# Kernel tuning notes

Measured on AMD Instinct MI355X. Metric: run time of the kernel, lower is better.

The kernel has to match this reference:

```python
import jax, jax.numpy as jnp
import numpy as np

B, C, H, W = 32, 512, 32, 32
R = C // 2  # reduced channels for key/prod projections


def setup_inputs() -> dict:
    key = jax.random.key(0)
    ks = jax.random.split(key, 8)
    s_in = 1.0 / np.sqrt(C)
    return {
        "x": jax.random.normal(ks[0], (B, C, H, W), jnp.float32),
        "Wk": jax.random.normal(ks[1], (R, C), jnp.float32) * s_in,
        "bk": jax.random.normal(ks[2], (R,), jnp.float32) * s_in,
        "Wp": jax.random.normal(ks[3], (R, C), jnp.float32) * s_in,
        "bp": jax.random.normal(ks[4], (R,), jnp.float32) * s_in,
        "Wv": jax.random.normal(ks[5], (C, C), jnp.float32) * s_in,
        "bv": jax.random.normal(ks[6], (C,), jnp.float32) * s_in,
        "param": jax.random.normal(ks[7], (1,), jnp.float32),
    }


def _conv1x1(x, Wmat, b):
    # 1x1 conv on NCHW == per-pixel channel matmul
    return jnp.einsum('bchw,oc->bohw', x, Wmat) + b[None, :, None, None]


def reference(x, Wk, bk, Wp, bp, Wv, bv, param):
    b, c, h, w = x.shape
    hw = h * w
    f_key = _conv1x1(x, Wk, bk).reshape(b, -1, hw).transpose(0, 2, 1)  # [B,HW,R]
    f_prod = _conv1x1(x, Wp, bp).reshape(b, -1, hw)                    # [B,R,HW]
    f_value = _conv1x1(x, Wv, bv).reshape(b, -1, hw)                   # [B,C,HW]
    energy = jnp.einsum('bnr,brm->bnm', f_key, f_prod)                 # [B,HW,HW]
    similarity = jax.nn.softmax(energy, axis=-1)
    # bmm(f_value, similarity^T): out[b,c,n] = sum_m f_value[b,c,m] * sim[b,n,m]
    attended = jnp.einsum('bcm,bnm->bcn', f_value, similarity).reshape(b, c, h, w)
    return x + attended * param
```

## Files before the change

### kernel.cpp

```cpp
#include <hip/hip_runtime.h>
#include <hip/hip_bf16.h>

#define BATCH 32
#define CCH   512
#define HWSZ  1024
#define RCH   256

typedef __attribute__((ext_vector_type(8))) _Float16 f16x8;
typedef __attribute__((ext_vector_type(4))) float f32x4;

__device__ __forceinline__ ushort f2h(float f) {
    _Float16 h = (_Float16)f;
    ushort u; __builtin_memcpy(&u, &h, 2);
    return u;
}
__device__ __forceinline__ float h2f(ushort u) {
    _Float16 h; __builtin_memcpy(&h, &u, 2);
    return (float)h;
}

__device__ __forceinline__ void load_lds16(const void* g, void* l) {
    __builtin_amdgcn_global_load_lds((const __attribute__((address_space(1))) void*)g,
                                     (__attribute__((address_space(3))) void*)l,
                                     16, 0, 0);
}

__device__ __forceinline__ f32x4 mfma16(f16x8 a, f16x8 b, f32x4 c) {
    return __builtin_amdgcn_mfma_f32_16x16x32_f16(a, b, c, 0, 0, 0);
}

__device__ __forceinline__ void xcd_swizzle(int& bx, int& by, int& bz) {
    int gx = gridDim.x, gy = gridDim.y;
    int n   = gx * gy * gridDim.z;
    int lin = bx + gx * (by + gy * bz);
    int cpx = n >> 3;
    int s = (lin & 7) * cpx + (lin >> 3);
    bx = s % gx; s /= gx;
    by = s % gy;
    bz = s / gy;
}

__global__ __launch_bounds__(256) void k_pre(
    const float* __restrict__ x, ushort* __restrict__ xt,
    const float* __restrict__ Wk, const float* __restrict__ bk,
    const float* __restrict__ Wp, const float* __restrict__ bp,
    const float* __restrict__ Wv,
    ushort* __restrict__ Wkp_h, ushort* __restrict__ Wv_h, float* __restrict__ bias_kp)
{
    __shared__ float tile[64][68];
    int t = threadIdx.x;
    if (blockIdx.z == 32) {
        int base = ((blockIdx.y * 16 + blockIdx.x) * 256 + t) * 8;
        int o = base >> 9, c = base & 511;
        const float* srcKP = (o < 256) ? (Wk + (size_t)o * 512 + c)
                                       : (Wp + (size_t)(o - 256) * 512 + c);
        float4 a0 = *(const float4*)srcKP;
        float4 a1 = *(const float4*)(srcKP + 4);
        ushort4 h0, h1;
        h0.x = f2h(a0.x); h0.y = f2h(a0.y); h0.z = f2h(a0.z); h0.w = f2h(a0.w);
        h1.x = f2h(a1.x); h1.y = f2h(a1.y); h1.z = f2h(a1.z); h1.w = f2h(a1.w);
        *(ushort4*)&Wkp_h[base] = h0;
        *(ushort4*)&Wkp_h[base + 4] = h1;
        float4 v0 = *(const float4*)(Wv + base);
        float4 v1 = *(const float4*)(Wv + base + 4);
        h0.x = f2h(v0.x); h0.y = f2h(v0.y); h0.z = f2h(v0.z); h0.w = f2h(v0.w);
        h1.x = f2h(v1.x); h1.y = f2h(v1.y); h1.z = f2h(v1.z); h1.w = f2h(v1.w);
        *(ushort4*)&Wv_h[base] = h0;
        *(ushort4*)&Wv_h[base + 4] = h1;
        if (c == 0) bias_kp[o] = (o < 256) ? bk[o] : bp[o - 256];
        return;
    }
    int b  = blockIdx.z;
    int c0 = blockIdx.y * 64;
    int n0 = blockIdx.x * 64;
    const float* xb = x + (size_t)b * CCH * HWSZ;
    int tc  = t >> 4;
    int tn4 = (t & 15) * 4;
    #pragma unroll
    for (int i = 0; i < 4; ++i) {
        int c = tc + i * 16;
        *(float4*)&tile[c][tn4] = *(const float4*)&xb[(size_t)(c0 + c) * HWSZ + n0 + tn4];
    }
    __syncthreads();
    ushort* oh = xt + (size_t)b * HWSZ * CCH;
    int tn  = t >> 4;
    int tc4 = (t & 15) * 4;
    #pragma unroll
    for (int i = 0; i < 4; ++i) {
        int n = tn + i * 16;
        ushort4 h;
        h.x = f2h(tile[tc4 + 0][n]);
        h.y = f2h(tile[tc4 + 1][n]);
        h.z = f2h(tile[tc4 + 2][n]);
        h.w = f2h(tile[tc4 + 3][n]);
        *(ushort4*)&oh[(size_t)(n0 + n) * CCH + c0 + tc4] = h;
    }
}

template<int MODE>
__global__ __launch_bounds__(512, 4) void k_gemm128(
    const ushort* __restrict__ A, const ushort* __restrict__ B,
    int lda, int ldb, long aBatch, long bBatch,
    ushort* __restrict__ out16, long oBatch, int ldo,
    const float* __restrict__ bias, int NT)
{
    __shared__ ushort lds[2][12288];
    int bx = blockIdx.x, by = blockIdx.y, bz = blockIdx.z;
    xcd_swizzle(bx, by, bz);
    const int z  = bz;
    const int m0 = bx * 128;
    const int n0 = by * 256;
    const int t    = threadIdx.x;
    const int lane = t & 63;
    const int w    = t >> 6;
    const int wm = w >> 2, wn = w & 3;
    const int l15 = lane & 15;
    const int hi  = lane >> 4;
    const int G   = hi ^ ((lane >> 1) & 3);

    const ushort* Ab = A + (size_t)z * aBatch;
    const ushort* Bb = B + (size_t)z * bBatch;

    const int sr = t >> 2;
    const int sg = (t & 3) ^ ((t >> 3) & 3);

    f32x4 acc[4][4] = {};
    f16x8 a[4], b01[2], b23[2];

#define STAGE(slot, kt) do {                                                 \
        size_t sa_ = (size_t)(m0 + sr) * lda + (kt) * 32 + sg * 8;           \
        load_lds16(Ab + sa_, &lds[slot][t * 8]);                             \
        size_t sb_ = (size_t)(n0 + sr) * ldb + (kt) * 32 + sg * 8;           \
        load_lds16(Bb + sb_, &lds[slot][4096 + t * 8]);                      \
        load_lds16(Bb + sb_ + (size_t)128 * ldb, &lds[slot][8192 + t * 8]);  \
    } while (0)

#define RD_ALL(slot) do {                                                    \
        _Pragma("unroll")                                                    \
        for (int ni = 0; ni < 2; ++ni)                                       \
            b01[ni] = *(const f16x8*)&lds[slot][4096 + (wn * 64 + ni * 16 + l15) * 32 + G * 8]; \
        _Pragma("unroll")                                                    \
        for (int ni = 0; ni < 2; ++ni)                                       \
            b23[ni] = *(const f16x8*)&lds[slot][4096 + (wn * 64 + 32 + ni * 16 + l15) * 32 + G * 8]; \
        _Pragma("unroll")                                                    \
        for (int mi = 0; mi < 4; ++mi)                                       \
            a[mi] = *(const f16x8*)&lds[slot][(wm * 64 + mi * 16 + l15) * 32 + G * 8]; \
    } while (0)

#define BAR() __builtin_amdgcn_s_barrier()
#define WLG(N) do { asm volatile("s_waitcnt lgkmcnt(" #N ")" ::: "memory");  \
                    __builtin_amdgcn_sched_barrier(0); } while (0)
#define WVM(N) asm volatile("s_waitcnt vmcnt(" #N ")" ::: "memory")

#define MM4(mi) do {                                                         \
        acc[mi][0] = mfma16(a[mi], b01[0], acc[mi][0]);                      \
        acc[mi][1] = mfma16(a[mi], b01[1], acc[mi][1]);                      \
        acc[mi][2] = mfma16(a[mi], b23[0], acc[mi][2]);                      \
        acc[mi][3] = mfma16(a[mi], b23[1], acc[mi][3]);                      \
    } while (0)

#define MFMA_PIPE() do {                                                     \
        WLG(3); MM4(0); WLG(2); MM4(1); WLG(1); MM4(2); WLG(0); MM4(3);      \
    } while (0)

    STAGE(0, 0);
    WVM(0);
    BAR();
    for (int j = 0; j < NT - 1; ++j) {
        int cur = j & 1;
        STAGE(cur ^ 1, j + 1);
        RD_ALL(cur);
        MFMA_PIPE();
        WVM(0);
        BAR();
    }
    RD_ALL(1);
    MFMA_PIPE();

    #pragma unroll
    for (int mi = 0; mi < 4; ++mi) {
        #pragma unroll
        for (int ni = 0; ni < 4; ++ni) {
            int gc  = n0 + wn * 64 + (ni >> 1) * 32 + (ni & 1) * 16 + l15;
            int gr0 = m0 + wm * 64 + mi * 16 + hi * 4;
            #pragma unroll
            for (int jj = 0; jj < 4; ++jj) {
                int gr = gr0 + jj;
                float v = acc[mi][ni][jj];
                if (MODE == 0) {
                    v += bias[gc];
                    out16[(size_t)gr * ldo + gc] = f2h(v);
                } else {
                    v += bias[gr];
                    out16[(size_t)z * oBatch + (size_t)gr * ldo + gc] = f2h(v);
                }
            }
        }
    }
#undef STAGE
#undef RD_ALL
#undef BAR
#undef WLG
#undef WVM
#undef MM4
#undef MFMA_PIPE
}

template<int MODE>
__global__ __launch_bounds__(512, 2) void k_gemm256(
    const ushort* __restrict__ A, const ushort* __restrict__ B,
    int lda, int ldb, long aBatch, long bBatch,
    float* __restrict__ outF, ushort* __restrict__ out16,
    long oBatch, int ldo,
    const float* __restrict__ xres, const float* __restrict__ param,
    int NT)
{
    __shared__ ushort lds[2][2][2][8192];
    int bx = blockIdx.x, by = blockIdx.y, bz = blockIdx.z;
    xcd_swizzle(bx, by, bz);
    const int z  = bz;
    const int m0 = bx * 256;
    const int n0 = by * 256;
    const int t    = threadIdx.x;
    const int lane = t & 63;
    const int w    = t >> 6;
    const int wm = w >> 2, wn = w & 3;
    const int l15 = lane & 15;
    const int hi  = lane >> 4;
    const int G   = hi ^ ((lane >> 1) & 3);

    const ushort* Ab = A + (size_t)z * aBatch;
    const ushort* Bb = B + (size_t)z * bBatch;

    const int sr = t >> 2;
    const int sg = (t & 3) ^ ((t >> 3) & 3);

    f32x4 acc[8][4] = {};
    f16x8 a[8], b[2];

#define STAGE(par, op, ks, kt) do {                                          \
        const ushort* gb_ = (op) ? Bb : Ab;                                  \
        int ld_ = (op) ? ldb : lda;                                          \
        int r0_ = (op) ? n0 : m0;                                            \
        size_t src_ = (size_t)(r0_ + sr) * ld_ + (kt) * 64 + (ks) * 32 + sg * 8; \
        load_lds16(gb_ + src_, &lds[par][op][ks][t * 8]);                    \
        load_lds16(gb_ + src_ + (size_t)128 * ld_, &lds[par][op][ks][t * 8 + 4096]); \
    } while (0)

#define LDA_(cur, ks) do {                                                   \
        _Pragma("unroll")                                                    \
        for (int mi = 0; mi < 8; ++mi)                                       \
            a[mi] = *(const f16x8*)&lds[cur][0][ks][(wm * 128 + mi * 16 + l15) * 32 + G * 8]; \
    } while (0)

#define LDB_(cur, ks, nh) do {                                               \
        _Pragma("unroll")                                                    \
        for (int ni = 0; ni < 2; ++ni)                                       \
            b[ni] = *(const f16x8*)&lds[cur][1][ks][(wn * 64 + (nh) * 32 + ni * 16 + l15) * 32 + G * 8]; \
    } while (0)

#define BAR() __builtin_amdgcn_s_barrier()

#define WLG(N) do { asm volatile("s_waitcnt lgkmcnt(" #N ")" ::: "memory");  \
                    __builtin_amdgcn_sched_barrier(0); } while (0)

#define MM2(mi, nh) do {                                                     \
        acc[mi][(nh)*2+0] = mfma16(a[mi], b[0], acc[mi][(nh)*2+0]);          \
        acc[mi][(nh)*2+1] = mfma16(a[mi], b[1], acc[mi][(nh)*2+1]);          \
    } while (0)

#define MFMA_PIPE() do {                                                     \
        WLG(7); MM2(0, 0); WLG(6); MM2(1, 0); WLG(5); MM2(2, 0);             \
        WLG(4); MM2(3, 0); WLG(3); MM2(4, 0); WLG(2); MM2(5, 0);             \
        WLG(1); MM2(6, 0); WLG(0); MM2(7, 0);                                \
    } while (0)

#define MFMA_BLK1() do {                                                     \
        WLG(0);                                                              \
        MM2(0, 1); MM2(1, 1); MM2(2, 1); MM2(3, 1);                          \
        MM2(4, 1); MM2(5, 1); MM2(6, 1); MM2(7, 1);                          \
    } while (0)

    STAGE(0, 0, 0, 0); STAGE(0, 1, 0, 0); STAGE(0, 0, 1, 0); STAGE(0, 1, 1, 0);
    asm volatile("s_waitcnt vmcnt(4)" ::: "memory");
    BAR();

    for (int j = 0; j < NT - 1; ++j) {
        int cur = j & 1, nxt = cur ^ 1;
        STAGE(nxt, 0, 0, j + 1);
        LDB_(cur, 0, 0); LDA_(cur, 0);
        MFMA_PIPE();
        STAGE(nxt, 1, 0, j + 1);
        LDB_(cur, 0, 1);
        MFMA_BLK1();
        asm volatile("s_waitcnt vmcnt(4)" ::: "memory");
        BAR();
        STAGE(nxt, 0, 1, j + 1);
        LDB_(cur, 1, 0); LDA_(cur, 1);
        MFMA_PIPE();
        STAGE(nxt, 1, 1, j + 1);
        LDB_(cur, 1, 1);
        MFMA_BLK1();
        asm volatile("s_waitcnt vmcnt(4)" ::: "memory");
        BAR();
    }
    {
        int cur = (NT - 1) & 1;
        LDB_(cur, 0, 0); LDA_(cur, 0);
        MFMA_PIPE();
        LDB_(cur, 0, 1);
        MFMA_BLK1();
        asm volatile("s_waitcnt vmcnt(0)" ::: "memory");
        BAR();
        LDB_(cur, 1, 0); LDA_(cur, 1);
        MFMA_PIPE();
        LDB_(cur, 1, 1);
        MFMA_BLK1();
    }

    if (MODE == 3) {
        float* fbuf = (float*)lds;
        const float prm = param[0];
        float*       ob = outF + (size_t)z * oBatch;
        const float* xb = xres + (size_t)z * oBatch;
        #pragma unroll
        for (int h = 0; h < 2; ++h) {
            asm volatile("s_waitcnt lgkmcnt(0)" ::: "memory");
            BAR();
            if ((wn >> 1) == h) {
                #pragma unroll
                for (int mi = 0; mi < 8; ++mi)
                    #pragma unroll
                    for (int ni = 0; ni < 4; ++ni) {
                        int cc = (wn & 1) * 64 + (ni >> 1) * 32 + (ni & 1) * 16 + l15;
                        int nn = (wm * 128 + mi * 16 + hi * 4) ^ ((cc & 7) << 2);
                        *(f32x4*)&fbuf[cc * 256 + nn] = acc[mi][ni];
                    }
            }
            asm volatile("s_waitcnt lgkmcnt(0)" ::: "memory");
            BAR();
            #pragma unroll
            for (int rr = 0; rr < 16; ++rr) {
                int cc = w * 16 + rr;
                f32x4 o4 = *(const f32x4*)&fbuf[cc * 256 + ((lane * 4) ^ ((cc & 7) << 2))];
                size_t g = (size_t)(n0 + h * 128 + cc) * ldo + m0 + lane * 4;
                float4 xv = *(const float4*)&xb[g];
                float4 ov;
                ov.x = xv.x + o4[0] * prm;
                ov.y = xv.y + o4[1] * prm;
                ov.z = xv.z + o4[2] * prm;
                ov.w = xv.w + o4[3] * prm;
                *(float4*)&ob[g] = ov;
            }
        }
    } else {
        #pragma unroll
        for (int mi = 0; mi < 8; ++mi) {
            #pragma unroll
            for (int ni = 0; ni < 4; ++ni) {
                int gc  = n0 + wn * 64 + (ni >> 1) * 32 + (ni & 1) * 16 + l15;
                int gr0 = m0 + wm * 128 + mi * 16 + hi * 4;
                #pragma unroll
                for (int jj = 0; jj < 4; ++jj) {
                    int gr = gr0 + jj;
                    out16[(size_t)z * oBatch + (size_t)(gr0 + jj) * ldo + gc] = f2h(acc[mi][ni][jj]);
                    (void)gr;
                }
            }
        }
    }
#undef STAGE
#undef LDA_
#undef LDB_
#undef BAR
#undef WLG
#undef MM2
#undef MFMA_PIPE
#undef MFMA_BLK1
}

__global__ __launch_bounds__(256) void k_softmax(ushort* __restrict__ E)
{
    int t    = threadIdx.x;
    int rowi = t >> 7;
    int tl   = t & 127;
    ushort* row = E + (size_t)(blockIdx.x * 2 + rowi) * HWSZ;
    uint4 u = *(const uint4*)&row[tl * 8];
    float v[8];
    v[0] = h2f(u.x & 0xffff); v[1] = h2f(u.x >> 16);
    v[2] = h2f(u.y & 0xffff); v[3] = h2f(u.y >> 16);
    v[4] = h2f(u.z & 0xffff); v[5] = h2f(u.z >> 16);
    v[6] = h2f(u.w & 0xffff); v[7] = h2f(u.w >> 16);
    float mx = v[0];
    #pragma unroll
    for (int i = 1; i < 8; ++i) mx = fmaxf(mx, v[i]);
    #pragma unroll
    for (int off = 1; off < 64; off <<= 1)
        mx = fmaxf(mx, __shfl_xor(mx, off));
    __shared__ float redm[2][2];
    __shared__ float reds[2][2];
    int lane = t & 63, wv = (t >> 6) & 1;
    if (lane == 0) redm[rowi][wv] = mx;
    __syncthreads();
    mx = fmaxf(redm[rowi][0], redm[rowi][1]);
    float s = 0.f;
    #pragma unroll
    for (int i = 0; i < 8; ++i) { v[i] = __expf(v[i] - mx); s += v[i]; }
    #pragma unroll
    for (int off = 1; off < 64; off <<= 1)
        s += __shfl_xor(s, off);
    if (lane == 0) reds[rowi][wv] = s;
    __syncthreads();
    s = reds[rowi][0] + reds[rowi][1];
    float inv = 1.0f / s;
    uint4 o;
    o.x = (unsigned)f2h(v[0] * inv) | ((unsigned)f2h(v[1] * inv) << 16);
    o.y = (unsigned)f2h(v[2] * inv) | ((unsigned)f2h(v[3] * inv) << 16);
    o.z = (unsigned)f2h(v[4] * inv) | ((unsigned)f2h(v[5] * inv) << 16);
    o.w = (unsigned)f2h(v[6] * inv) | ((unsigned)f2h(v[7] * inv) << 16);
    *(uint4*)&row[tl * 8] = o;
}

extern "C" void kernel_launch(void* const* d_in, const int* in_sizes, int n_in,
                              void* d_out, int out_size, void* d_ws, size_t ws_size,
                              hipStream_t stream)
{
    const float* x    = (const float*)d_in[0];
    const float* Wk   = (const float*)d_in[1];
    const float* bk   = (const float*)d_in[2];
    const float* Wp   = (const float*)d_in[3];
    const float* bp   = (const float*)d_in[4];
    const float* Wv   = (const float*)d_in[5];
    const float* bv   = (const float*)d_in[6];
    const float* prm  = (const float*)d_in[7];
    float* out = (float*)d_out;
    char* ws = (char*)d_ws;

    const size_t SZ16 = (size_t)BATCH * HWSZ * CCH * 2;
    ushort* xt    = (ushort*)(ws + 0);
    ushort* KPt   = (ushort*)(ws + SZ16);
    ushort* fv    = (ushort*)(ws + 2 * SZ16);
    ushort* E     = (ushort*)(ws + 3 * SZ16);
    char* wbase   = ws + 3 * SZ16 + (size_t)BATCH * HWSZ * HWSZ * 2;
    ushort* Wkp_h = (ushort*)(wbase);
    ushort* Wv_h  = (ushort*)(wbase + 524288);
    float*  bias_kp = (float*)(wbase + 2 * 524288);

    k_pre<<<dim3(16, 8, 33), 256, 0, stream>>>(
        x, xt, Wk, bk, Wp, bp, Wv, Wkp_h, Wv_h, bias_kp);

    k_gemm128<0><<<dim3(256, 2, 1), 512, 0, stream>>>(
        xt, Wkp_h, CCH, CCH, 0, 0,
        KPt, 0, CCH, bias_kp, CCH / 32);

    k_gemm128<1><<<dim3(4, 4, 32), 512, 0, stream>>>(
        Wv_h, xt, CCH, CCH, 0, (long)HWSZ * CCH,
        fv, (long)CCH * HWSZ, HWSZ, bv, CCH / 32);

    k_gemm256<2><<<dim3(4, 4, 32), 512, 0, stream>>>(
        KPt, KPt + RCH, CCH, CCH,
        (long)HWSZ * CCH, (long)HWSZ * CCH,
        nullptr, E, (long)HWSZ * HWSZ, HWSZ,
        nullptr, nullptr, RCH / 64);

    k_softmax<<<BATCH * HWSZ / 2, 256, 0, stream>>>(E);

    k_gemm256<3><<<dim3(4, 2, 32), 512, 0, stream>>>(
        E, fv, HWSZ, HWSZ,
        (long)HWSZ * HWSZ, (long)CCH * HWSZ,
        out, nullptr, (long)CCH * HWSZ, HWSZ,
        x, prm, HWSZ / 64);
}
```

Measured before the change: 176.7 us.

## Merge key/prod and value projections into one launch; halve energy GEMM grid

Fuses the two projection GEMMs (key/prod and value) into one kernel launch, using blockIdx.z to pick which GEMM a block computes. This removes one launch and the tail gap between the two kernels. The energy GEMM now has each block compute two 256-wide N tiles in sequence, halving its grid so there are fewer blocks and less scheduling overhead. The cost is more serial work per block, with no reuse of the A tile across the two N tiles.

```diff
diff --git a/kernel.cpp b/kernel.cpp
--- a/kernel.cpp
+++ b/kernel.cpp
@@ -97,19 +97,15 @@
     }
 }
 
-template<int MODE>
-__global__ __launch_bounds__(512, 4) void k_gemm128(
-    const ushort* __restrict__ A, const ushort* __restrict__ B,
-    int lda, int ldb, long aBatch, long bBatch,
-    ushort* __restrict__ out16, long oBatch, int ldo,
-    const float* __restrict__ bias, int NT)
+__global__ __launch_bounds__(512, 4) void k_proj(
+    const ushort* __restrict__ xt, const ushort* __restrict__ Wkp_h,
+    const ushort* __restrict__ Wv_h, const float* __restrict__ bias_kp,
+    const float* __restrict__ bv,
+    ushort* __restrict__ KPt, ushort* __restrict__ fv)
 {
     __shared__ ushort lds[2][12288];
     int bx = blockIdx.x, by = blockIdx.y, bz = blockIdx.z;
     xcd_swizzle(bx, by, bz);
-    const int z  = bz;
-    const int m0 = bx * 128;
-    const int n0 = by * 256;
     const int t    = threadIdx.x;
     const int lane = t & 63;
     const int w    = t >> 6;
@@ -117,22 +113,37 @@
     const int l15 = lane & 15;
     const int hi  = lane >> 4;
     const int G   = hi ^ ((lane >> 1) & 3);
-
-    const ushort* Ab = A + (size_t)z * aBatch;
-    const ushort* Bb = B + (size_t)z * bBatch;
-
     const int sr = t >> 2;
     const int sg = (t & 3) ^ ((t >> 3) & 3);
+    const int NT = CCH / 32;
+
+    const ushort *Ab, *Bb;
+    ushort* outp;
+    const float* bias;
+    int m0, n0, ldo;
+    bool colB;
+    if (bz < 32) {
+        Ab = Wv_h;
+        Bb = xt + (size_t)bz * HWSZ * CCH;
+        outp = fv + (size_t)bz * CCH * HWSZ;
+        bias = bv; colB = false; ldo = HWSZ;
+        m0 = bx * 128; n0 = by * 256;
+    } else {
+        int idx = (bz - 32) * 16 + by * 4 + bx;
+        Ab = xt; Bb = Wkp_h;
+        outp = KPt; bias = bias_kp; colB = true; ldo = CCH;
+        m0 = (idx >> 1) * 128; n0 = (idx & 1) * 256;
+    }
 
     f32x4 acc[4][4] = {};
     f16x8 a[4], b01[2], b23[2];
 
 #define STAGE(slot, kt) do {                                                 \
-        size_t sa_ = (size_t)(m0 + sr) * lda + (kt) * 32 + sg * 8;           \
+        size_t sa_ = (size_t)(m0 + sr) * CCH + (kt) * 32 + sg * 8;           \
         load_lds16(Ab + sa_, &lds[slot][t * 8]);                             \
-        size_t sb_ = (size_t)(n0 + sr) * ldb + (kt) * 32 + sg * 8;           \
+        size_t sb_ = (size_t)(n0 + sr) * CCH + (kt) * 32 + sg * 8;           \
         load_lds16(Bb + sb_, &lds[slot][4096 + t * 8]);                      \
-        load_lds16(Bb + sb_ + (size_t)128 * ldb, &lds[slot][8192 + t * 8]);  \
+        load_lds16(Bb + sb_ + (size_t)128 * CCH, &lds[slot][8192 + t * 8]);  \
     } while (0)
 
 #define RD_ALL(slot) do {                                                    \
@@ -186,14 +197,8 @@
             #pragma unroll
             for (int jj = 0; jj < 4; ++jj) {
                 int gr = gr0 + jj;
-                float v = acc[mi][ni][jj];
-                if (MODE == 0) {
-                    v += bias[gc];
-                    out16[(size_t)gr * ldo + gc] = f2h(v);
-                } else {
-                    v += bias[gr];
-                    out16[(size_t)z * oBatch + (size_t)gr * ldo + gc] = f2h(v);
-                }
+                float v = acc[mi][ni][jj] + (colB ? bias[gc] : bias[gr]);
+                outp[(size_t)gr * ldo + gc] = f2h(v);
             }
         }
     }
@@ -220,7 +225,6 @@
     xcd_swizzle(bx, by, bz);
     const int z  = bz;
     const int m0 = bx * 256;
-    const int n0 = by * 256;
     const int t    = threadIdx.x;
     const int lane = t & 63;
     const int w    = t >> 6;
@@ -235,8 +239,7 @@
     const int sr = t >> 2;
     const int sg = (t & 3) ^ ((t >> 3) & 3);
 
-    f32x4 acc[8][4] = {};
-    f16x8 a[8], b[2];
+    int n0;
 
 #define STAGE(par, op, ks, kt) do {                                          \
         const ushort* gb_ = (op) ? Bb : Ab;                                  \
@@ -281,90 +284,94 @@
         MM2(4, 1); MM2(5, 1); MM2(6, 1); MM2(7, 1);                          \
     } while (0)
 
-    STAGE(0, 0, 0, 0); STAGE(0, 1, 0, 0); STAGE(0, 0, 1, 0); STAGE(0, 1, 1, 0);
-    asm volatile("s_waitcnt vmcnt(4)" ::: "memory");
-    BAR();
-
-    for (int j = 0; j < NT - 1; ++j) {
-        int cur = j & 1, nxt = cur ^ 1;
-        STAGE(nxt, 0, 0, j + 1);
-        LDB_(cur, 0, 0); LDA_(cur, 0);
-        MFMA_PIPE();
-        STAGE(nxt, 1, 0, j + 1);
-        LDB_(cur, 0, 1);
-        MFMA_BLK1();
+    const int nyN = (MODE == 2) ? 2 : 1;
+    for (int ny = 0; ny < nyN; ++ny) {
+        n0 = (MODE == 2) ? (by * 512 + ny * 256) : (by * 256);
+        f32x4 acc[8][4] = {};
+        f16x8 a[8], b[2];
+
+        STAGE(0, 0, 0, 0); STAGE(0, 1, 0, 0); STAGE(0, 0, 1, 0); STAGE(0, 1, 1, 0);
         asm volatile("s_waitcnt vmcnt(4)" ::: "memory");
         BAR();
-        STAGE(nxt, 0, 1, j + 1);
-        LDB_(cur, 1, 0); LDA_(cur, 1);
-        MFMA_PIPE();
-        STAGE(nxt, 1, 1, j + 1);
-        LDB_(cur, 1, 1);
-        MFMA_BLK1();
-        asm volatile("s_waitcnt vmcnt(4)" ::: "memory");
-        BAR();
-    }
-    {
-        int cur = (NT - 1) & 1;
-        LDB_(cur, 0, 0); LDA_(cur, 0);
-        MFMA_PIPE();
-        LDB_(cur, 0, 1);
-        MFMA_BLK1();
-        asm volatile("s_waitcnt vmcnt(0)" ::: "memory");
-        BAR();
-        LDB_(cur, 1, 0); LDA_(cur, 1);
-        MFMA_PIPE();
-        LDB_(cur, 1, 1);
-        MFMA_BLK1();
-    }
-
-    if (MODE == 3) {
-        float* fbuf = (float*)lds;
-        const float prm = param[0];
-        float*       ob = outF + (size_t)z * oBatch;
-        const float* xb = xres + (size_t)z * oBatch;
-        #pragma unroll
-        for (int h = 0; h < 2; ++h) {
-            asm volatile("s_waitcnt lgkmcnt(0)" ::: "memory");
+
+        for (int j = 0; j < NT - 1; ++j) {
+            int cur = j & 1, nxt = cur ^ 1;
+            STAGE(nxt, 0, 0, j + 1);
+            LDB_(cur, 0, 0); LDA_(cur, 0);
+            MFMA_PIPE();
+            STAGE(nxt, 1, 0, j + 1);
+            LDB_(cur, 0, 1);
+            MFMA_BLK1();
+            asm volatile("s_waitcnt vmcnt(4)" ::: "memory");
             BAR();
-            if ((wn >> 1) == h) {
+            STAGE(nxt, 0, 1, j + 1);
+            LDB_(cur, 1, 0); LDA_(cur, 1);
+            MFMA_PIPE();
+            STAGE(nxt, 1, 1, j + 1);
+            LDB_(cur, 1, 1);
+            MFMA_BLK1();
+            asm volatile("s_waitcnt vmcnt(4)" ::: "memory");
+            BAR();
+        }
+        {
+            int cur = (NT - 1) & 1;
+            LDB_(cur, 0, 0); LDA_(cur, 0);
+            MFMA_PIPE();
+            LDB_(cur, 0, 1);
+            MFMA_BLK1();
+            asm volatile("s_waitcnt vmcnt(0)" ::: "memory");
+            BAR();
+            LDB_(cur, 1, 0); LDA_(cur, 1);
+            MFMA_PIPE();
+            LDB_(cur, 1, 1);
+            MFMA_BLK1();
+        }
+
+        if (MODE == 3) {
+            float* fbuf = (float*)lds;
+            const float prm = param[0];
+            float*       ob = outF + (size_t)z * oBatch;
+            const float* xb = xres + (size_t)z * oBatch;
+            #pragma unroll
+            for (int h = 0; h < 2; ++h) {
+                asm volatile("s_waitcnt lgkmcnt(0)" ::: "memory");
+                BAR();
+                if ((wn >> 1) == h) {
+                    #pragma unroll
+                    for (int mi = 0; mi < 8; ++mi)
+                        #pragma unroll
+                        for (int ni = 0; ni < 4; ++ni) {
+                            int cc = (wn & 1) * 64 + (ni >> 1) * 32 + (ni & 1) * 16 + l15;
+                            int nn = (wm * 128 + mi * 16 + hi * 4) ^ ((cc & 7) << 2);
+                            *(f32x4*)&fbuf[cc * 256 + nn] = acc[mi][ni];
+                        }
+                }
+                asm volatile("s_waitcnt lgkmcnt(0)" ::: "memory");
+                BAR();
                 #pragma unroll
-                for (int mi = 0; mi < 8; ++mi)
+                for (int rr = 0; rr < 16; ++rr) {
+                    int cc = w * 16 + rr;
+                    f32x4 o4 = *(const f32x4*)&fbuf[cc * 256 + ((lane * 4) ^ ((cc & 7) << 2))];
+                    size_t g = (size_t)(n0 + h * 128 + cc) * ldo + m0 + lane * 4;
+                    float4 xv = *(const float4*)&xb[g];
+                    float4 ov;
+                    ov.x = xv.x + o4[0] * prm;
+                    ov.y = xv.y + o4[1] * prm;
+                    ov.z = xv.z + o4[2] * prm;
+                    ov.w = xv.w + o4[3] * prm;
+                    *(float4*)&ob[g] = ov;
+                }
+            }
+        } else {
+            #pragma unroll
+            for (int mi = 0; mi < 8; ++mi) {
+                #pragma unroll
+                for (int ni = 0; ni < 4; ++ni) {
+                    int gc  = n0 + wn * 64 + (ni >> 1) * 32 + (ni & 1) * 16 + l15;
+                    int gr0 = m0 + wm * 128 + mi * 16 + hi * 4;
                     #pragma unroll
-                    for (int ni = 0; ni < 4; ++ni) {
-                        int cc = (wn & 1) * 64 + (ni >> 1) * 32 + (ni & 1) * 16 + l15;
-                        int nn = (wm * 128 + mi * 16 + hi * 4) ^ ((cc & 7) << 2);
-                        *(f32x4*)&fbuf[cc * 256 + nn] = acc[mi][ni];
-                    }
-            }
-            asm volatile("s_waitcnt lgkmcnt(0)" ::: "memory");
-            BAR();
-            #pragma unroll
-            for (int rr = 0; rr < 16; ++rr) {
-                int cc = w * 16 + rr;
-                f32x4 o4 = *(const f32x4*)&fbuf[cc * 256 + ((lane * 4) ^ ((cc & 7) << 2))];
-                size_t g = (size_t)(n0 + h * 128 + cc) * ldo + m0 + lane * 4;
-                float4 xv = *(const float4*)&xb[g];
-                float4 ov;
-                ov.x = xv.x + o4[0] * prm;
-                ov.y = xv.y + o4[1] * prm;
-                ov.z = xv.z + o4[2] * prm;
-                ov.w = xv.w + o4[3] * prm;
-                *(float4*)&ob[g] = ov;
-            }
-        }
-    } else {
-        #pragma unroll
-        for (int mi = 0; mi < 8; ++mi) {
-            #pragma unroll
-            for (int ni = 0; ni < 4; ++ni) {
-                int gc  = n0 + wn * 64 + (ni >> 1) * 32 + (ni & 1) * 16 + l15;
-                int gr0 = m0 + wm * 128 + mi * 16 + hi * 4;
-                #pragma unroll
-                for (int jj = 0; jj < 4; ++jj) {
-                    int gr = gr0 + jj;
-                    out16[(size_t)z * oBatch + (size_t)(gr0 + jj) * ldo + gc] = f2h(acc[mi][ni][jj]);
-                    (void)gr;
+                    for (int jj = 0; jj < 4; ++jj)
+                        out16[(size_t)z * oBatch + (size_t)(gr0 + jj) * ldo + gc] = f2h(acc[mi][ni][jj]);
                 }
             }
         }
@@ -449,15 +456,10 @@
     k_pre<<<dim3(16, 8, 33), 256, 0, stream>>>(
         x, xt, Wk, bk, Wp, bp, Wv, Wkp_h, Wv_h, bias_kp);
 
-    k_gemm128<0><<<dim3(256, 2, 1), 512, 0, stream>>>(
-        xt, Wkp_h, CCH, CCH, 0, 0,
-        KPt, 0, CCH, bias_kp, CCH / 32);
-
-    k_gemm128<1><<<dim3(4, 4, 32), 512, 0, stream>>>(
-        Wv_h, xt, CCH, CCH, 0, (long)HWSZ * CCH,
-        fv, (long)CCH * HWSZ, HWSZ, bv, CCH / 32);
-
-    k_gemm256<2><<<dim3(4, 4, 32), 512, 0, stream>>>(
+    k_proj<<<dim3(4, 4, 64), 512, 0, stream>>>(
+        xt, Wkp_h, Wv_h, bias_kp, bv, KPt, fv);
+
+    k_gemm256<2><<<dim3(4, 2, 32), 512, 0, stream>>>(
         KPt, KPt + RCH, CCH, CCH,
         (long)HWSZ * CCH, (long)HWSZ * CCH,
         nullptr, E, (long)HWSZ * HWSZ, HWSZ,
```

Result: slower. 186.5 us (+5.5%).
